# Performance work log

Hardware: AMD Instinct MI355X
Metric: run time of the kernel (lower is better)

The kernel has to match this reference:

```python
import jax, jax.numpy as jnp
import numpy as np

N_NODES = 50000; N_EDGES = 600000; N_GRAPHS = 128
IN_CH = 128; PROJ = 128; OUT_CH = 128; K = 3; NCLASS = 2; EPS = 1e-5


def _mask():
    # xhi_layer_mask: block i (rows i*OUT_CH:(i+1)*OUT_CH) sees first PROJ*(i+1) input cols
    blocks = []
    for i in range(K):
        m = np.zeros((OUT_CH, PROJ * K), np.float32)
        m[:, :PROJ * (i + 1)] = 1.0
        blocks.append(m)
    return jnp.asarray(np.concatenate(blocks, 0))


def _bn(x, g, b):
    # BatchNorm1d in training mode: biased batch stats, affine g/b
    m = jnp.mean(x, axis=0)
    v = jnp.var(x, axis=0)
    return (x - m) * jax.lax.rsqrt(v + EPS) * g + b


def setup_inputs() -> dict:
    key = jax.random.key(0)
    ks = jax.random.split(key, 10)
    M = OUT_CH * K
    def w(k, shape):
        return jax.random.normal(k, shape, jnp.float32) * 0.05
    return {
        "x": jax.random.normal(ks[0], (N_NODES, IN_CH), jnp.float32),
        "edge_index": jax.random.randint(ks[1], (2, N_EDGES), 0, N_NODES),
        "batch": jnp.sort(jax.random.randint(ks[2], (N_NODES,), 0, N_GRAPHS)),
        "n_graphs": N_GRAPHS,
        "w_rel": w(ks[3], (PROJ, IN_CH)), "b_rel": jnp.zeros((PROJ,), jnp.float32),
        "w_root": w(ks[4], (PROJ, IN_CH)),
        "norm0_g": jnp.ones((PROJ,), jnp.float32), "norm0_b": jnp.zeros((PROJ,), jnp.float32),
        "lin_w": w(ks[5], (M, PROJ * K)), "lin_b": jnp.zeros((M,), jnp.float32),
        "bnh_g": jnp.ones((M,), jnp.float32), "bnh_b": jnp.zeros((M,), jnp.float32),
        "bno_g": jnp.ones((3 * M,), jnp.float32), "bno_b": jnp.zeros((3 * M,), jnp.float32),
        "w1": w(ks[6], (2 * M, 3 * M)), "b1": jnp.zeros((2 * M,), jnp.float32),
        "w2": w(ks[7], (M, 2 * M)), "b2": jnp.zeros((M,), jnp.float32),
        "w3": w(ks[8], (NCLASS, M)), "b3": jnp.zeros((NCLASS,), jnp.float32),
    }


def reference(x, edge_index, batch, n_graphs, w_rel, b_rel, w_root, norm0_g, norm0_b,
              lin_w, lin_b, bnh_g, bnh_b, bno_g, bno_b, w1, b1, w2, b2, w3, b3):
    row, col = edge_index[0], edge_index[1]
    # GraphConv: lin_rel(sum_{j->i} x_j) + lin_root(x_i)
    neigh = jax.ops.segment_sum(x[row], col, num_segments=N_NODES)
    X = neigh @ w_rel.T + b_rel + x @ w_root.T
    X = _bn(X, norm0_g, norm0_b)
    # k-hop polynomial diffusion: A^i X computed as iterative SpMM over edges
    # (A[r,c] = 1 for edge (r,c): (A v)[r] = sum over edges of v[c])
    H = [X]
    cur = X
    for _ in range(K - 1):
        cur = jax.ops.segment_sum(cur[col], row, num_segments=N_NODES)
        H.append(cur)
    Hc = jnp.concatenate(H, axis=1)  # [N, PROJ*K]
    Hm = _bn(Hc @ (lin_w * _mask()).T + lin_b, bnh_g, bnh_b)  # [N, OUT_CH*K]
    # global mean / add / max pooling per graph
    ones = jnp.ones((N_NODES,), jnp.float32)
    cnt = jax.ops.segment_sum(ones, batch, num_segments=n_graphs)
    Hadd = jax.ops.segment_sum(Hm, batch, num_segments=n_graphs)
    Havg = Hadd / jnp.maximum(cnt, 1.0)[:, None]
    Hmax = jax.ops.segment_max(Hm, batch, num_segments=n_graphs)
    Hmax = jnp.where(jnp.isfinite(Hmax), Hmax, 0.0)  # guard empty segments
    Hcat = jnp.concatenate([Havg, Hadd, Hmax], axis=1)  # [G, 3*OUT_CH*K]
    # funnel readout (dropout = identity in eval)
    h = _bn(Hcat, bno_g, bno_b)
    h = jax.nn.relu(h @ w1.T + b1)
    h = jax.nn.relu(h @ w2.T + b2)
    return jax.nn.log_softmax(h @ w3.T + b3, axis=1)
```

## Files before the change

kernel.cpp:

```cpp
#include <hip/hip_runtime.h>
#include <math.h>

#define N_NODES 50000
#define N_EDGES 600000
#define N_GRAPHS 128
#define IN_CH 128
#define PROJ 128
#define OUT_CH 128
#define M_DIM 384
#define HC_DIM 384
#define CAT_DIM 1152
#define H1_DIM 768
#define EPS 1e-5f
#define SCAN_BLK 256
#define NPART 8
#define PART_NODES 6250
#define NPB 64

using bf16x8 = __attribute__((ext_vector_type(8))) short;
using f32x4  = __attribute__((ext_vector_type(4))) float;

__device__ inline unsigned short f2bf(float f) {
  unsigned u = __float_as_uint(f);
  unsigned r = u + 0x7fffu + ((u >> 16) & 1u);
  return (unsigned short)(r >> 16);
}
__device__ inline float bf2f(unsigned short h) {
  return __uint_as_float(((unsigned)h) << 16);
}

__device__ inline void atomicMaxF(float* addr, float val) {
  int iv = __float_as_int(val);
  if (iv >= 0) atomicMax((int*)addr, iv);
  else         atomicMin((unsigned int*)addr, (unsigned int)iv);
}
__device__ inline void atomicMinF(float* addr, float val) {
  int iv = __float_as_int(val);
  if (iv >= 0) atomicMin((int*)addr, iv);
  else         atomicMax((unsigned int*)addr, (unsigned int)iv);
}

__global__ void fill_minmax_kernel(float* __restrict__ gmax, float* __restrict__ gmin) {
  int i = blockIdx.x * blockDim.x + threadIdx.x;
  if (i < N_GRAPHS * M_DIM) {
    gmax[i] = -__builtin_inff();
    gmin[i] =  __builtin_inff();
  }
}

__global__ void bounds_kernel(const int* __restrict__ batch, int* __restrict__ start) {
  int i = blockIdx.x * blockDim.x + threadIdx.x;
  if (i >= N_NODES) return;
  int b = batch[i];
  int bp = (i == 0) ? -1 : batch[i - 1];
  for (int g = bp + 1; g <= b; ++g) start[g] = i;
  if (i == N_NODES - 1)
    for (int g = b + 1; g <= N_GRAPHS; ++g) start[g] = N_NODES;
}

__global__ void cnt_from_bounds_kernel(const int* __restrict__ start, float* __restrict__ cnt) {
  int g = threadIdx.x;
  if (g < N_GRAPHS) cnt[g] = (float)(start[g + 1] - start[g]);
}

__global__ __launch_bounds__(256) void hist_part_kernel(
    const int* __restrict__ row, const int* __restrict__ col,
    int* __restrict__ degA, int* __restrict__ degB) {
  const int part = blockIdx.x & (NPART - 1);
  const int slice = blockIdx.x >> 3;
  const int lo = part * PART_NODES, hi = lo + PART_NODES;
  for (int e = slice * 256 + threadIdx.x; e < N_EDGES; e += NPB * 256) {
    int r = row[e], c = col[e];
    if (c >= lo && c < hi) atomicAdd(&degA[c], 1);
    if (r >= lo && r < hi) atomicAdd(&degB[r], 1);
  }
}

__global__ __launch_bounds__(256) void fill_csr_part_kernel(
    const int* __restrict__ row, const int* __restrict__ col,
    int* __restrict__ cursA, int* __restrict__ eidxA,
    int* __restrict__ cursB, int* __restrict__ eidxB) {
  const int part = blockIdx.x & (NPART - 1);
  const int slice = blockIdx.x >> 3;
  const int lo = part * PART_NODES, hi = lo + PART_NODES;
  for (int e = slice * 256 + threadIdx.x; e < N_EDGES; e += NPB * 256) {
    int r = row[e], c = col[e];
    if (c >= lo && c < hi) eidxA[atomicAdd(&cursA[c], 1)] = r;
    if (r >= lo && r < hi) eidxB[atomicAdd(&cursB[r], 1)] = c;
  }
}

__global__ void scan1_kernel(const int* __restrict__ deg, int* __restrict__ offs,
                             int* __restrict__ bsum, int n) {
  __shared__ int sh[SCAN_BLK];
  int i = blockIdx.x * SCAN_BLK + threadIdx.x;
  int v = (i < n) ? deg[i] : 0;
  sh[threadIdx.x] = v; __syncthreads();
  #pragma unroll
  for (int d = 1; d < SCAN_BLK; d <<= 1) {
    int t = (threadIdx.x >= d) ? sh[threadIdx.x - d] : 0;
    __syncthreads();
    sh[threadIdx.x] += t;
    __syncthreads();
  }
  if (i < n) offs[i] = sh[threadIdx.x] - v;
  if (threadIdx.x == SCAN_BLK - 1) bsum[blockIdx.x] = sh[threadIdx.x];
}

__global__ void scan2_kernel(int* __restrict__ bsum, int nb) {
  __shared__ int sh[SCAN_BLK];
  int v = (threadIdx.x < nb) ? bsum[threadIdx.x] : 0;
  sh[threadIdx.x] = v; __syncthreads();
  #pragma unroll
  for (int d = 1; d < SCAN_BLK; d <<= 1) {
    int t = (threadIdx.x >= d) ? sh[threadIdx.x - d] : 0;
    __syncthreads();
    sh[threadIdx.x] += t;
    __syncthreads();
  }
  if (threadIdx.x < nb) bsum[threadIdx.x] = sh[threadIdx.x] - v;
}

__global__ void scan3_kernel(int* __restrict__ offs, const int* __restrict__ bsum,
                             int* __restrict__ cursor, int n) {
  int i = blockIdx.x * SCAN_BLK + threadIdx.x;
  if (i < n) {
    int o = offs[i] + bsum[blockIdx.x];
    offs[i] = o;
    cursor[i] = o;
  }
}

__global__ void convert_x_kernel(const float* __restrict__ x, unsigned short* __restrict__ xnb) {
  int t = blockIdx.x * blockDim.x + threadIdx.x;
  if (t >= N_NODES * 32) return;
  int node = t >> 5;
  int c4 = (t & 31) << 2;
  float4 v = *(const float4*)(x + (size_t)node * IN_CH + c4);
  ushort4 h = {f2bf(v.x), f2bf(v.y), f2bf(v.z), f2bf(v.w)};
  *(ushort4*)(xnb + (size_t)node * 256 + 128 + c4) = h;
}

__global__ void convert_wcat_kernel(const float* __restrict__ w_rel, const float* __restrict__ w_root,
                                    unsigned short* __restrict__ wcatb) {
  int t = blockIdx.x * blockDim.x + threadIdx.x;
  if (t >= 128 * 64) return;
  int n = t >> 6;
  int c4 = (t & 63) << 2;
  const float* src = (c4 < 128) ? (w_rel + (size_t)n * 128 + c4)
                                : (w_root + (size_t)n * 128 + (c4 - 128));
  float4 v = *(const float4*)src;
  ushort4 h = {f2bf(v.x), f2bf(v.y), f2bf(v.z), f2bf(v.w)};
  *(ushort4*)(wcatb + (size_t)n * 256 + c4) = h;
}

__global__ void convert_linw_kernel(const float* __restrict__ lin_w, unsigned short* __restrict__ linwb) {
  int t = blockIdx.x * blockDim.x + threadIdx.x;
  if (t >= 384 * 96) return;
  int n = t / 96;
  int c4 = (t - n * 96) << 2;
  float4 v = *(const float4*)(lin_w + (size_t)n * HC_DIM + c4);
  ushort4 h = {f2bf(v.x), f2bf(v.y), f2bf(v.z), f2bf(v.w)};
  *(ushort4*)(linwb + (size_t)n * HC_DIM + c4) = h;
}

__global__ __launch_bounds__(256) void gather_bf16_kernel(
    const unsigned short* __restrict__ src, const int* __restrict__ offs,
    const int* __restrict__ ends, const int* __restrict__ eidx,
    unsigned short* __restrict__ dst, int src_ld, int dst_ld) {
  int tid = blockIdx.x * blockDim.x + threadIdx.x;
  int node = tid >> 5;
  int c = (tid & 31) << 2;
  if (node >= N_NODES) return;
  int j = offs[node], end = ends[node];
  float ax = 0.f, ay = 0.f, az = 0.f, aw = 0.f;
  for (; j + 1 < end; j += 2) {
    int s0 = eidx[j], s1 = eidx[j + 1];
    ushort4 v0 = *(const ushort4*)(src + (size_t)s0 * src_ld + c);
    ushort4 v1 = *(const ushort4*)(src + (size_t)s1 * src_ld + c);
    ax += bf2f(v0.x); ay += bf2f(v0.y); az += bf2f(v0.z); aw += bf2f(v0.w);
    ax += bf2f(v1.x); ay += bf2f(v1.y); az += bf2f(v1.z); aw += bf2f(v1.w);
  }
  if (j < end) {
    int s0 = eidx[j];
    ushort4 v0 = *(const ushort4*)(src + (size_t)s0 * src_ld + c);
    ax += bf2f(v0.x); ay += bf2f(v0.y); az += bf2f(v0.z); aw += bf2f(v0.w);
  }
  ushort4 h = {f2bf(ax), f2bf(ay), f2bf(az), f2bf(aw)};
  *(ushort4*)(dst + (size_t)node * dst_ld + c) = h;
}

__device__ inline void stage_tile(const unsigned short* __restrict__ src, int src_ld,
                                  int row0, int k0, int max_rows,
                                  char* __restrict__ zone, int t) {
  int r = t >> 1;
  int half = t & 1;
  const char* p = (const char*)(src + (size_t)(row0 + r) * src_ld + k0) + half * 64;
  bool ok = (row0 + r) < max_rows;
  #pragma unroll
  for (int jj = 0; jj < 4; ++jj) {
    uint4 v = make_uint4(0u, 0u, 0u, 0u);
    if (ok) v = *(const uint4*)(p + jj * 16);
    int slot = half * 4 + jj;
    *(uint4*)(zone + r * 128 + ((slot ^ (r & 7)) << 4)) = v;
  }
}

__device__ inline bf16x8 frag_ld(const char* __restrict__ zone, int row, int slot) {
  return *(const bf16x8*)(zone + row * 128 + ((slot ^ (row & 7)) << 4));
}

__global__ __launch_bounds__(256) void gemm_conv_mfma(
    const unsigned short* __restrict__ xnb, const unsigned short* __restrict__ wcatb,
    const float* __restrict__ b_rel, float* __restrict__ Hc0) {
  __shared__ char smem[32768];
  char* zoneA = smem;
  char* zoneB = smem + 16384;
  const int bm = blockIdx.x * 128;
  const int t = threadIdx.x;
  const int l = t & 63;
  const int wid = t >> 6;
  const int wr = wid >> 1, wc = wid & 1;
  const int lrow = l & 15, lk = l >> 4;
  f32x4 acc[4][4];
  #pragma unroll
  for (int i = 0; i < 4; ++i)
    #pragma unroll
    for (int jn = 0; jn < 4; ++jn) acc[i][jn] = (f32x4){0.f, 0.f, 0.f, 0.f};
  for (int st = 0; st < 4; ++st) {
    __syncthreads();
    stage_tile(xnb, 256, bm, st * 64, N_NODES, zoneA, t);
    stage_tile(wcatb, 256, 0, st * 64, 1 << 30, zoneB, t);
    __syncthreads();
    #pragma unroll
    for (int kk = 0; kk < 2; ++kk) {
      bf16x8 af[4], bfr[4];
      #pragma unroll
      for (int mf = 0; mf < 4; ++mf) af[mf] = frag_ld(zoneA, wr * 64 + mf * 16 + lrow, kk * 4 + lk);
      #pragma unroll
      for (int nf = 0; nf < 4; ++nf) bfr[nf] = frag_ld(zoneB, wc * 64 + nf * 16 + lrow, kk * 4 + lk);
      #pragma unroll
      for (int mf = 0; mf < 4; ++mf)
        #pragma unroll
        for (int nf = 0; nf < 4; ++nf)
          acc[mf][nf] = __builtin_amdgcn_mfma_f32_16x16x32_bf16(af[mf], bfr[nf], acc[mf][nf], 0, 0, 0);
    }
  }
  float brv[4];
  #pragma unroll
  for (int nf = 0; nf < 4; ++nf) brv[nf] = b_rel[wc * 64 + nf * 16 + lrow];
  #pragma unroll
  for (int mf = 0; mf < 4; ++mf) {
    #pragma unroll
    for (int q = 0; q < 4; ++q) {
      int r = bm + wr * 64 + mf * 16 + lk * 4 + q;
      if (r < N_NODES) {
        #pragma unroll
        for (int nf = 0; nf < 4; ++nf)
          Hc0[(size_t)r * 128 + wc * 64 + nf * 16 + lrow] = acc[mf][nf][q] + brv[nf];
      }
    }
  }
}

__global__ __launch_bounds__(256) void gemm_mask_mfma(
    const unsigned short* __restrict__ Hcb, const unsigned short* __restrict__ linwb,
    const float* __restrict__ lin_b, const int* __restrict__ batch,
    float* __restrict__ gsum, float* __restrict__ gmax, float* __restrict__ gmin,
    float* __restrict__ colsumsq) {
  __shared__ char smem[33792];
  __shared__ int bsh[128];
  char* zoneA = smem;
  char* zoneB = smem + 16384;
  const int bm = blockIdx.x * 128;
  const int bn = blockIdx.y * 128;
  const int nstages = 2 * (blockIdx.y + 1);
  const int t = threadIdx.x;
  const int l = t & 63;
  const int wid = t >> 6;
  const int wr = wid >> 1, wc = wid & 1;
  const int lrow = l & 15, lk = l >> 4;
  f32x4 acc[4][4];
  #pragma unroll
  for (int i = 0; i < 4; ++i)
    #pragma unroll
    for (int jn = 0; jn < 4; ++jn) acc[i][jn] = (f32x4){0.f, 0.f, 0.f, 0.f};
  for (int st = 0; st < nstages; ++st) {
    __syncthreads();
    stage_tile(Hcb, HC_DIM, bm, st * 64, N_NODES, zoneA, t);
    stage_tile(linwb, HC_DIM, bn, st * 64, 1 << 30, zoneB, t);
    __syncthreads();
    #pragma unroll
    for (int kk = 0; kk < 2; ++kk) {
      bf16x8 af[4], bfr[4];
      #pragma unroll
      for (int mf = 0; mf < 4; ++mf) af[mf] = frag_ld(zoneA, wr * 64 + mf * 16 + lrow, kk * 4 + lk);
      #pragma unroll
      for (int nf = 0; nf < 4; ++nf) bfr[nf] = frag_ld(zoneB, wc * 64 + nf * 16 + lrow, kk * 4 + lk);
      #pragma unroll
      for (int mf = 0; mf < 4; ++mf)
        #pragma unroll
        for (int nf = 0; nf < 4; ++nf)
          acc[mf][nf] = __builtin_amdgcn_mfma_f32_16x16x32_bf16(af[mf], bfr[nf], acc[mf][nf], 0, 0, 0);
    }
  }
  float lbv[4];
  #pragma unroll
  for (int nf = 0; nf < 4; ++nf) lbv[nf] = lin_b[bn + wc * 64 + nf * 16 + lrow];
  if (t < 128) bsh[t] = (bm + t < N_NODES) ? batch[bm + t] : -1;
  float* Y = (float*)smem;
  const int col = t & 127;
  const int gcol = bn + col;
  const int r0 = (t >> 7) * 32;
  float sq = 0.f;
  __syncthreads();
  for (int half = 0; half < 2; ++half) {
    if (wr == half) {
      #pragma unroll
      for (int mf = 0; mf < 4; ++mf)
        #pragma unroll
        for (int q = 0; q < 4; ++q) {
          int rr = mf * 16 + lk * 4 + q;
          #pragma unroll
          for (int nf = 0; nf < 4; ++nf)
            Y[rr * 132 + wc * 64 + nf * 16 + lrow] = acc[mf][nf][q] + lbv[nf];
        }
    }
    __syncthreads();
    int curg = -1;
    float s = 0.f, mx = 0.f, mn = 0.f;
    for (int rr = 0; rr < 32; ++rr) {
      int g = bsh[half * 64 + r0 + rr];
      if (g < 0) break;
      float y = Y[(r0 + rr) * 132 + col];
      sq += y * y;
      if (g != curg) {
        if (curg >= 0) {
          atomicAdd(&gsum[curg * M_DIM + gcol], s);
          atomicMaxF(&gmax[curg * M_DIM + gcol], mx);
          atomicMinF(&gmin[curg * M_DIM + gcol], mn);
        }
        curg = g; s = y; mx = y; mn = y;
      } else {
        s += y; mx = fmaxf(mx, y); mn = fminf(mn, y);
      }
    }
    if (curg >= 0) {
      atomicAdd(&gsum[curg * M_DIM + gcol], s);
      atomicMaxF(&gmax[curg * M_DIM + gcol], mx);
      atomicMinF(&gmin[curg * M_DIM + gcol], mn);
    }
    __syncthreads();
  }
  atomicAdd(&colsumsq[gcol], sq);
}

__global__ __launch_bounds__(256) void colstats0_kernel(
    const float* __restrict__ Hc0, float* __restrict__ colsum0, float* __restrict__ colsumsq0) {
  __shared__ float sh[256];
  int c = threadIdx.x & 127;
  int h = threadIdx.x >> 7;
  int r0 = blockIdx.x * 256;
  int rend = min(r0 + 256, N_NODES);
  float s = 0.f, q = 0.f;
  for (int r = r0 + h; r < rend; r += 2) {
    float v = Hc0[(size_t)r * 128 + c];
    s += v; q += v * v;
  }
  sh[threadIdx.x] = s; __syncthreads();
  if (h == 0) atomicAdd(&colsum0[c], sh[c] + sh[c + 128]);
  __syncthreads();
  sh[threadIdx.x] = q; __syncthreads();
  if (h == 0) atomicAdd(&colsumsq0[c], sh[c] + sh[c + 128]);
}

__global__ __launch_bounds__(256) void bn_apply0_kernel(
    const float* __restrict__ Hc0, unsigned short* __restrict__ Hcb,
    const float* __restrict__ colsum0, const float* __restrict__ colsumsq0,
    const float* __restrict__ g_, const float* __restrict__ b_) {
  int tid = blockIdx.x * blockDim.x + threadIdx.x;
  if (tid >= N_NODES * 32) return;
  int r = tid >> 5;
  int c = (tid & 31) << 2;
  float4 v = *(const float4*)(Hc0 + (size_t)r * 128 + c);
  float vv[4] = {v.x, v.y, v.z, v.w};
  #pragma unroll
  for (int j = 0; j < 4; ++j) {
    float m = colsum0[c + j] * (1.0f / N_NODES);
    float var = colsumsq0[c + j] * (1.0f / N_NODES) - m * m;
    float s = g_[c + j] * rsqrtf(var + EPS);
    float tt = b_[c + j] - m * s;
    vv[j] = vv[j] * s + tt;
  }
  ushort4 hh = {f2bf(vv[0]), f2bf(vv[1]), f2bf(vv[2]), f2bf(vv[3])};
  *(ushort4*)(Hcb + (size_t)r * HC_DIM + c) = hh;
}

__device__ inline float block_sum128(float v, float* red) {
  int t = threadIdx.x;
  red[t] = v; __syncthreads();
  #pragma unroll
  for (int s = 64; s >= 1; s >>= 1) {
    if (t < s) red[t] += red[t + s];
    __syncthreads();
  }
  float r = red[0];
  __syncthreads();
  return r;
}

__device__ inline void bn_write_col(float v, int col, const float* __restrict__ bg,
                                    const float* __restrict__ bb, float* __restrict__ h0T,
                                    float* red) {
  float s1 = block_sum128(v, red);
  float s2 = block_sum128(v * v, red);
  float m = s1 * (1.0f / N_GRAPHS);
  float var = s2 * (1.0f / N_GRAPHS) - m * m;
  float sc = bg[col] * rsqrtf(var + EPS);
  h0T[(size_t)col * N_GRAPHS + threadIdx.x] = (v - m) * sc + bb[col];
}

__global__ __launch_bounds__(128) void finalize_kernel(
    const float* __restrict__ gsum, const float* __restrict__ gmax,
    const float* __restrict__ gmin, const float* __restrict__ colsumsq,
    const float* __restrict__ cnt, const float* __restrict__ bnh_g,
    const float* __restrict__ bnh_b, const float* __restrict__ bno_g,
    const float* __restrict__ bno_b, float* __restrict__ h0T) {
  __shared__ float red[128];
  int c = blockIdx.x;
  int g = threadIdx.x;
  float vsum = gsum[g * M_DIM + c];
  float colsum = block_sum128(vsum, red);
  float m = colsum * (1.0f / N_NODES);
  float var = colsumsq[c] * (1.0f / N_NODES) - m * m;
  float s = bnh_g[c] * rsqrtf(var + EPS);
  float t = bnh_b[c] - m * s;
  float cg = cnt[g];
  float hadd = s * vsum + cg * t;
  float havg = hadd / fmaxf(cg, 1.0f);
  float hmax = 0.f;
  if (cg > 0.f)
    hmax = (s >= 0.f ? s * gmax[g * M_DIM + c] : s * gmin[g * M_DIM + c]) + t;
  bn_write_col(havg, c,        bno_g, bno_b, h0T, red);
  bn_write_col(hadd, 384 + c,  bno_g, bno_b, h0T, red);
  bn_write_col(hmax, 768 + c,  bno_g, bno_b, h0T, red);
}

__global__ __launch_bounds__(128) void mlp_kernel(
    const float* __restrict__ inT, const float* __restrict__ W,
    const float* __restrict__ bias, float* __restrict__ outT, int Kdim, int do_relu) {
  __shared__ float wrow[CAT_DIM];
  int oc = blockIdx.x;
  int g = threadIdx.x;
  for (int k = g; k < Kdim; k += 128) wrow[k] = W[(size_t)oc * Kdim + k];
  __syncthreads();
  float acc = bias[oc];
  for (int k = 0; k < Kdim; ++k) acc += inT[(size_t)k * N_GRAPHS + g] * wrow[k];
  if (do_relu) acc = fmaxf(acc, 0.f);
  outT[(size_t)oc * N_GRAPHS + g] = acc;
}

__global__ __launch_bounds__(128) void head_kernel(
    const float* __restrict__ h2T, const float* __restrict__ w3,
    const float* __restrict__ b3, float* __restrict__ out) {
  int g = threadIdx.x;
  float z0 = b3[0], z1 = b3[1];
  for (int k = 0; k < M_DIM; ++k) {
    float v = h2T[(size_t)k * N_GRAPHS + g];
    z0 += v * w3[k];
    z1 += v * w3[M_DIM + k];
  }
  float mz = fmaxf(z0, z1);
  float lse = mz + logf(expf(z0 - mz) + expf(z1 - mz));
  out[g * 2 + 0] = z0 - lse;
  out[g * 2 + 1] = z1 - lse;
}

extern "C" void kernel_launch(void* const* d_in, const int* in_sizes, int n_in,
                              void* d_out, int out_size, void* d_ws, size_t ws_size,
                              hipStream_t stream) {
  const float* x       = (const float*)d_in[0];
  const int*   row     = (const int*)d_in[1];
  const int*   col     = row + N_EDGES;
  const int*   batch   = (const int*)d_in[2];
  const float* w_rel   = (const float*)d_in[4];
  const float* b_rel   = (const float*)d_in[5];
  const float* w_root  = (const float*)d_in[6];
  const float* norm0_g = (const float*)d_in[7];
  const float* norm0_b = (const float*)d_in[8];
  const float* lin_w   = (const float*)d_in[9];
  const float* lin_b   = (const float*)d_in[10];
  const float* bnh_g   = (const float*)d_in[11];
  const float* bnh_b   = (const float*)d_in[12];
  const float* bno_g   = (const float*)d_in[13];
  const float* bno_b   = (const float*)d_in[14];
  const float* w1      = (const float*)d_in[15];
  const float* b1      = (const float*)d_in[16];
  const float* w2      = (const float*)d_in[17];
  const float* b2      = (const float*)d_in[18];
  const float* w3      = (const float*)d_in[19];
  const float* b3      = (const float*)d_in[20];
  float* out = (float*)d_out;

  char* ws = (char*)d_ws;
  size_t off = 0;
  auto allocb = [&](size_t nbytes) {
    char* p = ws + off;
    off += ((nbytes + 255) & ~(size_t)255);
    return p;
  };
  int*   degA      = (int*)allocb(N_NODES * 4);
  int*   degB      = (int*)allocb(N_NODES * 4);
  float* gsum      = (float*)allocb((size_t)N_GRAPHS * M_DIM * 4);
  float* colsumsq  = (float*)allocb(M_DIM * 4);
  float* colsum0   = (float*)allocb(PROJ * 4);
  float* colsumsq0 = (float*)allocb(PROJ * 4);
  size_t zero_bytes = off;
  float* cnt   = (float*)allocb(N_GRAPHS * 4);
  int*   gstart = (int*)allocb((N_GRAPHS + 1) * 4);
  int*   offsA = (int*)allocb(N_NODES * 4);
  int*   cursA = (int*)allocb(N_NODES * 4);
  int*   offsB = (int*)allocb(N_NODES * 4);
  int*   cursB = (int*)allocb(N_NODES * 4);
  int*   bsumA = (int*)allocb(SCAN_BLK * 4);
  int*   bsumB = (int*)allocb(SCAN_BLK * 4);
  int*   eidxA = (int*)allocb(N_EDGES * 4);
  int*   eidxB = (int*)allocb(N_EDGES * 4);
  float* Hc0   = (float*)allocb((size_t)N_NODES * 128 * 4);
  unsigned short* Hcb   = (unsigned short*)allocb((size_t)N_NODES * HC_DIM * 2);
  unsigned short* xnb   = (unsigned short*)allocb((size_t)N_NODES * 256 * 2);
  unsigned short* wcatb = (unsigned short*)allocb(128 * 256 * 2);
  unsigned short* linwb = (unsigned short*)allocb(384 * 384 * 2);
  float* gmax  = (float*)allocb((size_t)N_GRAPHS * M_DIM * 4);
  float* gmin  = (float*)allocb((size_t)N_GRAPHS * M_DIM * 4);
  float* h0T   = (float*)allocb((size_t)CAT_DIM * N_GRAPHS * 4);
  float* h1T   = (float*)allocb((size_t)H1_DIM * N_GRAPHS * 4);
  float* h2T   = (float*)allocb((size_t)M_DIM * N_GRAPHS * 4);

  const int NB = (N_NODES + SCAN_BLK - 1) / SCAN_BLK;

  hipMemsetAsync(d_ws, 0, zero_bytes, stream);
  fill_minmax_kernel<<<(N_GRAPHS * M_DIM + 255) / 256, 256, 0, stream>>>(gmax, gmin);
  bounds_kernel<<<(N_NODES + 255) / 256, 256, 0, stream>>>(batch, gstart);
  cnt_from_bounds_kernel<<<1, 128, 0, stream>>>(gstart, cnt);

  hist_part_kernel<<<NPART * NPB, 256, 0, stream>>>(row, col, degA, degB);
  scan1_kernel<<<NB, SCAN_BLK, 0, stream>>>(degA, offsA, bsumA, N_NODES);
  scan1_kernel<<<NB, SCAN_BLK, 0, stream>>>(degB, offsB, bsumB, N_NODES);
  scan2_kernel<<<1, SCAN_BLK, 0, stream>>>(bsumA, NB);
  scan2_kernel<<<1, SCAN_BLK, 0, stream>>>(bsumB, NB);
  scan3_kernel<<<NB, SCAN_BLK, 0, stream>>>(offsA, bsumA, cursA, N_NODES);
  scan3_kernel<<<NB, SCAN_BLK, 0, stream>>>(offsB, bsumB, cursB, N_NODES);
  fill_csr_part_kernel<<<NPART * NPB, 256, 0, stream>>>(row, col, cursA, eidxA, cursB, eidxB);

  convert_x_kernel<<<(N_NODES * 32 + 255) / 256, 256, 0, stream>>>(x, xnb);
  convert_wcat_kernel<<<(128 * 64 + 255) / 256, 256, 0, stream>>>(w_rel, w_root, wcatb);
  convert_linw_kernel<<<(384 * 96 + 255) / 256, 256, 0, stream>>>(lin_w, linwb);

  gather_bf16_kernel<<<(N_NODES * 32 + 255) / 256, 256, 0, stream>>>(
      xnb + 128, offsA, cursA, eidxA, xnb, 256, 256);
  gemm_conv_mfma<<<dim3((N_NODES + 127) / 128, 1), 256, 0, stream>>>(xnb, wcatb, b_rel, Hc0);
  colstats0_kernel<<<(N_NODES + 255) / 256, 256, 0, stream>>>(Hc0, colsum0, colsumsq0);
  bn_apply0_kernel<<<(N_NODES * 32 + 255) / 256, 256, 0, stream>>>(Hc0, Hcb, colsum0, colsumsq0, norm0_g, norm0_b);
  gather_bf16_kernel<<<(N_NODES * 32 + 255) / 256, 256, 0, stream>>>(
      Hcb, offsB, cursB, eidxB, Hcb + 128, HC_DIM, HC_DIM);
  gather_bf16_kernel<<<(N_NODES * 32 + 255) / 256, 256, 0, stream>>>(
      Hcb + 128, offsB, cursB, eidxB, Hcb + 256, HC_DIM, HC_DIM);
  gemm_mask_mfma<<<dim3((N_NODES + 127) / 128, 3), 256, 0, stream>>>(
      Hcb, linwb, lin_b, batch, gsum, gmax, gmin, colsumsq);
  finalize_kernel<<<M_DIM, 128, 0, stream>>>(gsum, gmax, gmin, colsumsq, cnt,
                                             bnh_g, bnh_b, bno_g, bno_b, h0T);
  mlp_kernel<<<H1_DIM, 128, 0, stream>>>(h0T, w1, b1, h1T, CAT_DIM, 1);
  mlp_kernel<<<M_DIM, 128, 0, stream>>>(h1T, w2, b2, h2T, H1_DIM, 1);
  head_kernel<<<1, 128, 0, stream>>>(h2T, w3, b3, out);
}
```

Measured before the change: 455.7 us.

## Fuse BN0 column stats into conv GEMM and stage tiles with global_load_lds

Computes the per-column sum and sum of squares for the first BatchNorm in the conv GEMM epilogue. It reduces them in LDS and then atomically adds into 8 striped copies, which a tiny bn_prep kernel combines into scale and shift. This removes the separate colstats pass that re-read Hc0, and stops bn_apply0 from recomputing the statistics for every element. GEMM tile staging now uses direct global-to-LDS async loads with an inverse swizzle instead of going through registers, and the masked GEMM grid is flattened so the longest-K column blocks launch first. The staging drops the row bounds check, so the last row tile reads past the valid rows into adjacent pool memory; only masked outputs depend on those rows.

```diff
diff --git a/kernel.cpp b/kernel.cpp
--- a/kernel.cpp
+++ b/kernel.cpp
@@ -16,6 +16,7 @@
 #define NPART 8
 #define PART_NODES 6250
 #define NPB 64
+#define NROWB 391
 
 using bf16x8 = __attribute__((ext_vector_type(8))) short;
 using f32x4  = __attribute__((ext_vector_type(4))) float;
@@ -38,6 +39,12 @@
   int iv = __float_as_int(val);
   if (iv >= 0) atomicMin((int*)addr, iv);
   else         atomicMax((unsigned int*)addr, (unsigned int)iv);
+}
+
+__device__ inline void gld16(const void* g, void* l) {
+  __builtin_amdgcn_global_load_lds(
+      (const __attribute__((address_space(1))) void*)g,
+      (__attribute__((address_space(3))) void*)l, 16, 0, 0);
 }
 
 __global__ void fill_minmax_kernel(float* __restrict__ gmax, float* __restrict__ gmin) {
@@ -190,19 +197,17 @@
   *(ushort4*)(dst + (size_t)node * dst_ld + c) = h;
 }
 
-__device__ inline void stage_tile(const unsigned short* __restrict__ src, int src_ld,
-                                  int row0, int k0, int max_rows,
-                                  char* __restrict__ zone, int t) {
-  int r = t >> 1;
-  int half = t & 1;
-  const char* p = (const char*)(src + (size_t)(row0 + r) * src_ld + k0) + half * 64;
-  bool ok = (row0 + r) < max_rows;
-  #pragma unroll
-  for (int jj = 0; jj < 4; ++jj) {
-    uint4 v = make_uint4(0u, 0u, 0u, 0u);
-    if (ok) v = *(const uint4*)(p + jj * 16);
-    int slot = half * 4 + jj;
-    *(uint4*)(zone + r * 128 + ((slot ^ (r & 7)) << 4)) = v;
+__device__ inline void stage_async(const unsigned short* __restrict__ src, int src_ld,
+                                   int row0, int k0, char* __restrict__ zone, int t) {
+  #pragma unroll
+  for (int p = 0; p < 4; ++p) {
+    int idx = p * 256 + t;
+    int r = idx >> 3;
+    int slot = idx & 7;
+    int sslot = slot ^ (r & 7);
+    const char* g = (const char*)(src + (size_t)(row0 + r) * src_ld + k0) + (sslot << 4);
+    void* l = zone + p * 4096 + (t >> 6) * 1024;
+    gld16(g, l);
   }
 }
 
@@ -212,7 +217,8 @@
 
 __global__ __launch_bounds__(256) void gemm_conv_mfma(
     const unsigned short* __restrict__ xnb, const unsigned short* __restrict__ wcatb,
-    const float* __restrict__ b_rel, float* __restrict__ Hc0) {
+    const float* __restrict__ b_rel, float* __restrict__ Hc0,
+    float* __restrict__ colsum8, float* __restrict__ colsq8) {
   __shared__ char smem[32768];
   char* zoneA = smem;
   char* zoneB = smem + 16384;
@@ -229,8 +235,8 @@
     for (int jn = 0; jn < 4; ++jn) acc[i][jn] = (f32x4){0.f, 0.f, 0.f, 0.f};
   for (int st = 0; st < 4; ++st) {
     __syncthreads();
-    stage_tile(xnb, 256, bm, st * 64, N_NODES, zoneA, t);
-    stage_tile(wcatb, 256, 0, st * 64, 1 << 30, zoneB, t);
+    stage_async(xnb, 256, bm, st * 64, zoneA, t);
+    stage_async(wcatb, 256, 0, st * 64, zoneB, t);
     __syncthreads();
     #pragma unroll
     for (int kk = 0; kk < 2; ++kk) {
@@ -261,6 +267,45 @@
       }
     }
   }
+  __syncthreads();
+  float* csum = (float*)smem;
+  float* csq  = (float*)(smem + 512);
+  if (t < 128) { csum[t] = 0.f; csq[t] = 0.f; }
+  __syncthreads();
+  #pragma unroll
+  for (int nf = 0; nf < 4; ++nf) {
+    int ccol = wc * 64 + nf * 16 + lrow;
+    float s = 0.f, q = 0.f;
+    #pragma unroll
+    for (int mf = 0; mf < 4; ++mf)
+      #pragma unroll
+      for (int qq = 0; qq < 4; ++qq) {
+        int r = bm + wr * 64 + mf * 16 + lk * 4 + qq;
+        if (r < N_NODES) { float v = acc[mf][nf][qq] + brv[nf]; s += v; q += v * v; }
+      }
+    atomicAdd(&csum[ccol], s);
+    atomicAdd(&csq[ccol], q);
+  }
+  __syncthreads();
+  if (t < 128) {
+    int cpy = (blockIdx.x & 7) * 128;
+    atomicAdd(&colsum8[cpy + t], csum[t]);
+    atomicAdd(&colsq8[cpy + t], csq[t]);
+  }
+}
+
+__global__ void bn_prep_kernel(const float* __restrict__ colsum8, const float* __restrict__ colsq8,
+                               const float* __restrict__ g_, const float* __restrict__ b_,
+                               float* __restrict__ bn_s, float* __restrict__ bn_t) {
+  int c = threadIdx.x;
+  float s1 = 0.f, s2 = 0.f;
+  #pragma unroll
+  for (int k = 0; k < 8; ++k) { s1 += colsum8[k * 128 + c]; s2 += colsq8[k * 128 + c]; }
+  float m = s1 * (1.0f / N_NODES);
+  float var = s2 * (1.0f / N_NODES) - m * m;
+  float sc = g_[c] * rsqrtf(var + EPS);
+  bn_s[c] = sc;
+  bn_t[c] = b_[c] - m * sc;
 }
 
 __global__ __launch_bounds__(256) void gemm_mask_mfma(
@@ -272,9 +317,11 @@
   __shared__ int bsh[128];
   char* zoneA = smem;
   char* zoneB = smem + 16384;
-  const int bm = blockIdx.x * 128;
-  const int bn = blockIdx.y * 128;
-  const int nstages = 2 * (blockIdx.y + 1);
+  const int bid = blockIdx.x;
+  const int ybl = 2 - bid / NROWB;
+  const int bm = (bid % NROWB) * 128;
+  const int bn = ybl * 128;
+  const int nstages = 2 * (ybl + 1);
   const int t = threadIdx.x;
   const int l = t & 63;
   const int wid = t >> 6;
@@ -287,8 +334,8 @@
     for (int jn = 0; jn < 4; ++jn) acc[i][jn] = (f32x4){0.f, 0.f, 0.f, 0.f};
   for (int st = 0; st < nstages; ++st) {
     __syncthreads();
-    stage_tile(Hcb, HC_DIM, bm, st * 64, N_NODES, zoneA, t);
-    stage_tile(linwb, HC_DIM, bn, st * 64, 1 << 30, zoneB, t);
+    stage_async(Hcb, HC_DIM, bm, st * 64, zoneA, t);
+    stage_async(linwb, HC_DIM, bn, st * 64, zoneB, t);
     __syncthreads();
     #pragma unroll
     for (int kk = 0; kk < 2; ++kk) {
@@ -355,29 +402,9 @@
   atomicAdd(&colsumsq[gcol], sq);
 }
 
-__global__ __launch_bounds__(256) void colstats0_kernel(
-    const float* __restrict__ Hc0, float* __restrict__ colsum0, float* __restrict__ colsumsq0) {
-  __shared__ float sh[256];
-  int c = threadIdx.x & 127;
-  int h = threadIdx.x >> 7;
-  int r0 = blockIdx.x * 256;
-  int rend = min(r0 + 256, N_NODES);
-  float s = 0.f, q = 0.f;
-  for (int r = r0 + h; r < rend; r += 2) {
-    float v = Hc0[(size_t)r * 128 + c];
-    s += v; q += v * v;
-  }
-  sh[threadIdx.x] = s; __syncthreads();
-  if (h == 0) atomicAdd(&colsum0[c], sh[c] + sh[c + 128]);
-  __syncthreads();
-  sh[threadIdx.x] = q; __syncthreads();
-  if (h == 0) atomicAdd(&colsumsq0[c], sh[c] + sh[c + 128]);
-}
-
 __global__ __launch_bounds__(256) void bn_apply0_kernel(
     const float* __restrict__ Hc0, unsigned short* __restrict__ Hcb,
-    const float* __restrict__ colsum0, const float* __restrict__ colsumsq0,
-    const float* __restrict__ g_, const float* __restrict__ b_) {
+    const float* __restrict__ bn_s, const float* __restrict__ bn_t) {
   int tid = blockIdx.x * blockDim.x + threadIdx.x;
   if (tid >= N_NODES * 32) return;
   int r = tid >> 5;
@@ -385,13 +412,8 @@
   float4 v = *(const float4*)(Hc0 + (size_t)r * 128 + c);
   float vv[4] = {v.x, v.y, v.z, v.w};
   #pragma unroll
-  for (int j = 0; j < 4; ++j) {
-    float m = colsum0[c + j] * (1.0f / N_NODES);
-    float var = colsumsq0[c + j] * (1.0f / N_NODES) - m * m;
-    float s = g_[c + j] * rsqrtf(var + EPS);
-    float tt = b_[c + j] - m * s;
-    vv[j] = vv[j] * s + tt;
-  }
+  for (int j = 0; j < 4; ++j)
+    vv[j] = vv[j] * bn_s[c + j] + bn_t[c + j];
   ushort4 hh = {f2bf(vv[0]), f2bf(vv[1]), f2bf(vv[2]), f2bf(vv[3])};
   *(ushort4*)(Hcb + (size_t)r * HC_DIM + c) = hh;
 }
@@ -513,11 +535,13 @@
   int*   degB      = (int*)allocb(N_NODES * 4);
   float* gsum      = (float*)allocb((size_t)N_GRAPHS * M_DIM * 4);
   float* colsumsq  = (float*)allocb(M_DIM * 4);
-  float* colsum0   = (float*)allocb(PROJ * 4);
-  float* colsumsq0 = (float*)allocb(PROJ * 4);
+  float* colsum8   = (float*)allocb(8 * PROJ * 4);
+  float* colsq8    = (float*)allocb(8 * PROJ * 4);
   size_t zero_bytes = off;
-  float* cnt   = (float*)allocb(N_GRAPHS * 4);
+  float* cnt    = (float*)allocb(N_GRAPHS * 4);
   int*   gstart = (int*)allocb((N_GRAPHS + 1) * 4);
+  float* bn_s   = (float*)allocb(PROJ * 4);
+  float* bn_t   = (float*)allocb(PROJ * 4);
   int*   offsA = (int*)allocb(N_NODES * 4);
   int*   cursA = (int*)allocb(N_NODES * 4);
   int*   offsB = (int*)allocb(N_NODES * 4);
@@ -559,14 +583,14 @@
 
   gather_bf16_kernel<<<(N_NODES * 32 + 255) / 256, 256, 0, stream>>>(
       xnb + 128, offsA, cursA, eidxA, xnb, 256, 256);
-  gemm_conv_mfma<<<dim3((N_NODES + 127) / 128, 1), 256, 0, stream>>>(xnb, wcatb, b_rel, Hc0);
-  colstats0_kernel<<<(N_NODES + 255) / 256, 256, 0, stream>>>(Hc0, colsum0, colsumsq0);
-  bn_apply0_kernel<<<(N_NODES * 32 + 255) / 256, 256, 0, stream>>>(Hc0, Hcb, colsum0, colsumsq0, norm0_g, norm0_b);
+  gemm_conv_mfma<<<NROWB, 256, 0, stream>>>(xnb, wcatb, b_rel, Hc0, colsum8, colsq8);
+  bn_prep_kernel<<<1, 128, 0, stream>>>(colsum8, colsq8, norm0_g, norm0_b, bn_s, bn_t);
+  bn_apply0_kernel<<<(N_NODES * 32 + 255) / 256, 256, 0, stream>>>(Hc0, Hcb, bn_s, bn_t);
   gather_bf16_kernel<<<(N_NODES * 32 + 255) / 256, 256, 0, stream>>>(
       Hcb, offsB, cursB, eidxB, Hcb + 128, HC_DIM, HC_DIM);
   gather_bf16_kernel<<<(N_NODES * 32 + 255) / 256, 256, 0, stream>>>(
       Hcb + 128, offsB, cursB, eidxB, Hcb + 256, HC_DIM, HC_DIM);
-  gemm_mask_mfma<<<dim3((N_NODES + 127) / 128, 3), 256, 0, stream>>>(
+  gemm_mask_mfma<<<NROWB * 3, 256, 0, stream>>>(
       Hcb, linwb, lin_b, batch, gsum, gmax, gmin, colsumsq);
   finalize_kernel<<<M_DIM, 128, 0, stream>>>(gsum, gmax, gmin, colsumsq, cnt,
                                              bnh_g, bnh_b, bno_g, bno_b, h0T);
```

Measured after the change: 419.2 us. 1.09x faster.
